# Kernel tuning notes

Measured on AMD Instinct MI355X. Metric: run time of the kernel, lower is better.

Reference implementation:

```python
import jax, jax.numpy as jnp
import numpy as np

H = 8        # num_heads
D = 128      # attention_dim
DV = 128     # linear_dim
B = 8
MAX_SEQLEN = 1024
LENGTHS = np.array([512 + 64 * b for b in range(B)], dtype=np.int64)  # jagged lengths
TOTAL = int(LENGTHS.sum())  # 5888


def setup_inputs() -> dict:
    key = jax.random.key(0)
    k1, k2, k3 = jax.random.split(key, 3)
    offsets = jnp.asarray(np.concatenate([[0], np.cumsum(LENGTHS)]), dtype=jnp.int32)
    tq = jax.random.normal(k1, (TOTAL, H * D), dtype=jnp.float32)
    tk = jax.random.normal(k2, (TOTAL, H * D), dtype=jnp.float32)
    tv = jax.random.normal(k3, (TOTAL, H * DV), dtype=jnp.float32)
    return {"tq": tq, "tk": tk, "tv": tv, "offsets": offsets,
            "max_seqlen": MAX_SEQLEN, "scaling_seqlen": -1}


def reference(tq, tk, tv, offsets, max_seqlen, scaling_seqlen):
    # HSTU jagged causal attention: out = (silu(q k^T * alpha) / n) @ v, per sequence.
    alpha = 1.0 / (D ** 0.5)
    denom = float(scaling_seqlen) if scaling_seqlen > 0 else float(max_seqlen)
    lengths = offsets[1:] - offsets[:-1]            # [B]
    pos = jnp.arange(max_seqlen, dtype=offsets.dtype)
    valid = pos[None, :] < lengths[:, None]          # [B, N] padding mask
    tok = offsets[:-1, None] + pos[None, :]          # [B, N] flat token index
    safe = jnp.where(valid, tok, 0)
    # gather jagged -> padded dense [B, N, H, D]
    q = tq.reshape(-1, H, D)[safe]
    k = tk.reshape(-1, H, D)[safe]
    v = tv.reshape(-1, H, DV)[safe]
    scores = jnp.einsum('bihd,bjhd->bhij', q, k) * alpha   # [B, H, N, N]
    attn = jax.nn.silu(scores) / denom                     # no softmax in HSTU
    causal = pos[:, None] >= pos[None, :]                  # attend to j <= i
    mask = causal[None, None, :, :] & valid[:, None, None, :] & valid[:, None, :, None]
    attn = jnp.where(mask, attn, 0.0)
    out = jnp.einsum('bhij,bjhd->bihd', attn, v)           # [B, N, H, DV]
    out = out * valid[:, :, None, None]
    # scatter padded -> jagged flat (invalid rows contribute zeros to index 0)
    flat = jnp.zeros((tq.shape[0], H, DV), tq.dtype).at[safe.reshape(-1)].add(
        out.reshape(-1, H, DV))
    return flat.reshape(-1, H * DV)
```

## Files before the change

kernel.cpp:

```cpp
#include <hip/hip_runtime.h>
#include <hip/hip_bf16.h>

typedef float f32x4 __attribute__((ext_vector_type(4)));
typedef __bf16 bf16x8 __attribute__((ext_vector_type(8)));
typedef unsigned int u32;
typedef unsigned int u32x2 __attribute__((ext_vector_type(2)));
typedef unsigned int u32x4 __attribute__((ext_vector_type(4)));
typedef unsigned short u16;

#define NH 8
#define HD 128
#define ROWE 1024
#define QB 64
#define JB 32
#define JCH 256
#define RSTRIDE 192
#define KSTR 148
#define VSTR 36
#define KSZ (JB*KSTR)
#define VSZ (HD*VSTR)

static __device__ __forceinline__ u16 bfb(float f) {
  return __builtin_bit_cast(u16, __float2bfloat16(f));
}
static __device__ __forceinline__ u32 pk2(float lo, float hi) {
  return (u32)bfb(lo) | ((u32)bfb(hi) << 16);
}

union FR { u32 u[4]; bf16x8 v; };

__global__ __launch_bounds__(256) void prep_cvt(
    const float* __restrict__ tk, const float* __restrict__ tv,
    u16* __restrict__ kb, u16* __restrict__ vb,
    float* __restrict__ outz, long n8)
{
  long idx = (long)blockIdx.x * 256 + threadIdx.x;
  long stride = (long)gridDim.x * 256;
  for (long i = idx; i < n8; i += stride) {
    const f32x4* kp = (const f32x4*)(tk + i * 8);
    const f32x4* vp = (const f32x4*)(tv + i * 8);
    f32x4 k0 = kp[0], k1 = kp[1], v0 = vp[0], v1 = vp[1];
    u32x4 ko, vo;
    ko.x = pk2(k0.x, k0.y); ko.y = pk2(k0.z, k0.w);
    ko.z = pk2(k1.x, k1.y); ko.w = pk2(k1.z, k1.w);
    vo.x = pk2(v0.x, v0.y); vo.y = pk2(v0.z, v0.w);
    vo.z = pk2(v1.x, v1.y); vo.w = pk2(v1.z, v1.w);
    *(u32x4*)(kb + i * 8) = ko;
    *(u32x4*)(vb + i * 8) = vo;
    f32x4 z = {0.f, 0.f, 0.f, 0.f};
    ((f32x4*)(outz + i * 8))[0] = z;
    ((f32x4*)(outz + i * 8))[1] = z;
  }
}

static __device__ __forceinline__ void unit_cj(int u, int& c, int& j) {
  c = (u & 3) | (((u >> 4) & 7) << 2);
  j = ((u >> 2) & 3) | (((u >> 7) & 7) << 2);
}

struct StReg { u32x2 k[4]; u32x2 v[4]; };

static __device__ __forceinline__ void stage_load(StReg& s,
    const u16* __restrict__ kb, const u16* __restrict__ vb,
    int base_row, int cap, int hoff, int tid) {
#pragma unroll
  for (int it = 0; it < 4; ++it) {
    int c, j; unit_cj(tid + (it << 8), c, j);
    int row = base_row + j; if (row > cap) row = cap;
    size_t g = (size_t)row * ROWE + hoff + 4 * c;
    s.k[it] = *(const u32x2*)(kb + g);
    s.v[it] = *(const u32x2*)(vb + g);
  }
}

static __device__ __forceinline__ void stage_write(const StReg& s,
    u16* kw, u16* vw, int tid) {
#pragma unroll
  for (int it = 0; it < 4; ++it) {
    int c, j; unit_cj(tid + (it << 8), c, j);
    *(u32x2*)(&kw[j * KSTR + 4 * c]) = s.k[it];
    u32x2 vv = s.v[it];
    vw[(4 * c + 0) * VSTR + j] = (u16)(vv.x);
    vw[(4 * c + 1) * VSTR + j] = (u16)(vv.x >> 16);
    vw[(4 * c + 2) * VSTR + j] = (u16)(vv.y);
    vw[(4 * c + 3) * VSTR + j] = (u16)(vv.y >> 16);
  }
}

__global__ __launch_bounds__(256, 3) void hstu_fwd(
    const u16* __restrict__ kb, const u16* __restrict__ vb,
    const float* __restrict__ tq, const int* __restrict__ offs,
    const int* __restrict__ pms, const int* __restrict__ pss,
    float* __restrict__ out, int nrows)
{
  __shared__ __align__(16) u16 kbuf[2][KSZ];
  __shared__ __align__(16) u16 vbuf[2][VSZ];

  const int h = blockIdx.x & 7;
  const int rblk = blockIdx.x >> 3;
  const int rstr = gridDim.x >> 3;

  int o[9];
#pragma unroll
  for (int i = 0; i < 9; ++i) o[i] = offs[i];

  const int cap = nrows - 1;
  const int tid = threadIdx.x;
  const int lane = tid & 63;
  const int w = tid >> 6;
  const int lrow = lane & 15;
  const int lgrp = lane >> 4;
  const int hoff = h * HD;

  const float qscale = 0.12751744f;
  int ms = pms[0], ss = pss[0];
  float den = (ss > 0) ? (float)ss : (float)ms;
  const float cs = 0.69314718056f / den;

  for (int e = rblk; ; e += rstr) {
    int r = e, selq = -1, selc = 0, soff = 0, sn = 0;
    for (int k = 15; k >= 0; --k) {
      for (int b = 0; b < 8; ++b) {
        int n = o[b + 1] - o[b];
        if (k * 64 >= n) continue;
        int je = k * 64 + 64; if (je > n) je = n;
        int nc = (je + JCH - 1) >> 8;
        if (r < nc) { selq = k; selc = r; soff = o[b]; sn = n; k = -1; break; }
        r -= nc;
      }
    }
    if (selq < 0) break;

    const int q0 = selq * QB;
    int jend = q0 + QB; if (jend > sn) jend = sn;
    const int ncq = (jend + JCH - 1) >> 8;
    const bool direct = (ncq == 1);
    const int j0c = selc * JCH;
    int jec = j0c + JCH; if (jec > jend) jec = jend;
    const int ntt = (jec - j0c + JB - 1) >> 5;

    FR qf[4];
    {
      int qr = soff + q0 + 16 * w + lrow; if (qr > cap) qr = cap;
      const float* qp = tq + (size_t)qr * ROWE + hoff;
#pragma unroll
      for (int ds = 0; ds < 4; ++ds) {
        f32x4 a = *(const f32x4*)(qp + ds * 32 + 4 * lgrp);
        f32x4 b = *(const f32x4*)(qp + ds * 32 + 4 * lgrp + 16);
        qf[ds].u[0] = pk2(a.x * qscale, a.y * qscale);
        qf[ds].u[1] = pk2(a.z * qscale, a.w * qscale);
        qf[ds].u[2] = pk2(b.x * qscale, b.y * qscale);
        qf[ds].u[3] = pk2(b.z * qscale, b.w * qscale);
      }
    }

    f32x4 acc[8];
#pragma unroll
    for (int i = 0; i < 8; ++i) acc[i] = (f32x4){0.f, 0.f, 0.f, 0.f};

    const int iq = q0 + 16 * w + lrow;

    __syncthreads();
    StReg st;
    stage_load(st, kb, vb, soff + j0c, cap, hoff, tid);
    stage_write(st, kbuf[0], vbuf[0], tid);

    for (int tt = 0; tt < ntt; ++tt) {
      __syncthreads();
      const bool pre = (tt + 1 < ntt);
      if (pre) stage_load(st, kb, vb, soff + j0c + (tt + 1) * JB, cap, hoff, tid);

      const int j0 = j0c + tt * JB;
      const int bsel = tt & 1;

      if (iq - lrow + 15 >= j0) {
        const char* kbc = (const char*)kbuf[bsel] + lrow * (2 * KSTR) + lgrp * 8;
        f32x4 s0 = {0.f, 0.f, 0.f, 0.f}, s1 = {0.f, 0.f, 0.f, 0.f};
#pragma unroll
        for (int ds = 0; ds < 4; ++ds) {
          FR a0, a1;
          const char* p = kbc + ds * 64;
          *(u32x2*)(&a0.u[0]) = *(const u32x2*)(p);
          *(u32x2*)(&a0.u[2]) = *(const u32x2*)(p + 32);
          *(u32x2*)(&a1.u[0]) = *(const u32x2*)(p + 16 * 2 * KSTR);
          *(u32x2*)(&a1.u[2]) = *(const u32x2*)(p + 16 * 2 * KSTR + 32);
          s0 = __builtin_amdgcn_mfma_f32_16x16x32_bf16(a0.v, qf[ds].v, s0, 0, 0, 0);
          s1 = __builtin_amdgcn_mfma_f32_16x16x32_bf16(a1.v, qf[ds].v, s1, 0, 0, 0);
        }

        const int jb0 = j0 + 4 * lgrp;
        float pv[8];
#pragma unroll
        for (int rr = 0; rr < 4; ++rr) {
          float y0 = s0[rr], y1 = s1[rr];
          float z0 = __fdividef(y0, 1.f + exp2f(-y0));
          float z1 = __fdividef(y1, 1.f + exp2f(-y1));
          pv[rr]     = (jb0 + rr      <= iq) ? z0 : 0.f;
          pv[rr + 4] = (jb0 + 16 + rr <= iq) ? z1 : 0.f;
        }
        FR pf;
        pf.u[0] = pk2(pv[0], pv[1]); pf.u[1] = pk2(pv[2], pv[3]);
        pf.u[2] = pk2(pv[4], pv[5]); pf.u[3] = pk2(pv[6], pv[7]);

        const char* vbc = (const char*)vbuf[bsel] + lrow * (2 * VSTR) + lgrp * 8;
#pragma unroll
        for (int sd = 0; sd < 8; ++sd) {
          FR vf;
          const char* p2 = vbc + sd * (16 * 2 * VSTR);
          *(u32x2*)(&vf.u[0]) = *(const u32x2*)(p2);
          *(u32x2*)(&vf.u[2]) = *(const u32x2*)(p2 + 32);
          acc[sd] = __builtin_amdgcn_mfma_f32_16x16x32_bf16(pf.v, vf.v, acc[sd], 0, 0, 0);
        }
      }
      if (pre) stage_write(st, kbuf[(tt + 1) & 1], vbuf[(tt + 1) & 1], tid);
    }

    const int or0 = q0 + 16 * w + 4 * lgrp;
#pragma unroll
    for (int rr = 0; rr < 4; ++rr) {
      int ir = or0 + rr;
      if (ir < sn) {
        float* op = out + (size_t)(soff + ir) * ROWE + hoff + lrow;
        if (direct) {
#pragma unroll
          for (int sd = 0; sd < 8; ++sd) op[sd * 16] = acc[sd][rr] * cs;
        } else {
#pragma unroll
          for (int sd = 0; sd < 8; ++sd)
            __hip_atomic_fetch_add(&op[sd * 16], acc[sd][rr] * cs,
                                   __ATOMIC_RELAXED, __HIP_MEMORY_SCOPE_AGENT);
        }
      }
    }
  }
}

extern "C" void kernel_launch(void* const* d_in, const int* in_sizes, int n_in,
                              void* d_out, int out_size, void* d_ws, size_t ws_size,
                              hipStream_t stream) {
  const float* tq = (const float*)d_in[0];
  const float* tk = (const float*)d_in[1];
  const float* tv = (const float*)d_in[2];
  const int* offs = (const int*)d_in[3];
  const int* pms  = (const int*)d_in[4];
  const int* pss  = (const int*)d_in[5];
  float* out = (float*)d_out;

  int nrows = in_sizes[0] / ROWE;
  u16* kbw = (u16*)d_ws;
  u16* vbw = kbw + (size_t)nrows * ROWE;
  long n8 = (long)nrows * ROWE / 8;

  hipLaunchKernelGGL(prep_cvt, dim3(2048), dim3(256), 0, stream,
                     tk, tv, kbw, vbw, out, n8);
  hipLaunchKernelGGL(hstu_fwd, dim3(NH * RSTRIDE), dim3(256), 0, stream,
                     kbw, vbw, tq, offs, pms, pss, out, nrows);
}
```

Baseline: 176.4 us.

## Use head-major K and transposed V, one wave per 16-row strip without LDS

The prep kernel now writes K in a head-major bf16 layout and V transposed per head (staged through LDS). It no longer zeroes the output. The attention kernel gives each wave its own 16-query strip, loads K and V fragments straight from global memory, and drops the LDS double-buffering, block barriers, the column-chunk split and the atomic accumulation. This removes synchronisation and atomics, but the four waves of a block no longer share K/V tiles, which raises global/L2 traffic and exposes load latency without explicit prefetch. It also assumes every sequence length is a multiple of 16.

```diff
diff --git a/kernel.cpp b/kernel.cpp
--- a/kernel.cpp
+++ b/kernel.cpp
@@ -11,14 +11,8 @@
 #define NH 8
 #define HD 128
 #define ROWE 1024
-#define QB 64
 #define JB 32
-#define JCH 256
-#define RSTRIDE 192
-#define KSTR 148
-#define VSTR 36
-#define KSZ (JB*KSTR)
-#define VSZ (HD*VSTR)
+#define VSTR2 72
 
 static __device__ __forceinline__ u16 bfb(float f) {
   return __builtin_bit_cast(u16, __float2bfloat16(f));
@@ -27,211 +21,166 @@
   return (u32)bfb(lo) | ((u32)bfb(hi) << 16);
 }
 
-union FR { u32 u[4]; bf16x8 v; };
+union FR { u32 u[4]; u32x4 q; bf16x8 v; };
 
 __global__ __launch_bounds__(256) void prep_cvt(
     const float* __restrict__ tk, const float* __restrict__ tv,
-    u16* __restrict__ kb, u16* __restrict__ vb,
-    float* __restrict__ outz, long n8)
+    u16* __restrict__ kb, u16* __restrict__ vt, int nrows)
 {
-  long idx = (long)blockIdx.x * 256 + threadIdx.x;
-  long stride = (long)gridDim.x * 256;
-  for (long i = idx; i < n8; i += stride) {
-    const f32x4* kp = (const f32x4*)(tk + i * 8);
-    const f32x4* vp = (const f32x4*)(tv + i * 8);
-    f32x4 k0 = kp[0], k1 = kp[1], v0 = vp[0], v1 = vp[1];
-    u32x4 ko, vo;
-    ko.x = pk2(k0.x, k0.y); ko.y = pk2(k0.z, k0.w);
-    ko.z = pk2(k1.x, k1.y); ko.w = pk2(k1.z, k1.w);
-    vo.x = pk2(v0.x, v0.y); vo.y = pk2(v0.z, v0.w);
-    vo.z = pk2(v1.x, v1.y); vo.w = pk2(v1.z, v1.w);
-    *(u32x4*)(kb + i * 8) = ko;
-    *(u32x4*)(vb + i * 8) = vo;
-    f32x4 z = {0.f, 0.f, 0.f, 0.f};
-    ((f32x4*)(outz + i * 8))[0] = z;
-    ((f32x4*)(outz + i * 8))[1] = z;
-  }
-}
-
-static __device__ __forceinline__ void unit_cj(int u, int& c, int& j) {
-  c = (u & 3) | (((u >> 4) & 7) << 2);
-  j = ((u >> 2) & 3) | (((u >> 7) & 7) << 2);
-}
-
-struct StReg { u32x2 k[4]; u32x2 v[4]; };
-
-static __device__ __forceinline__ void stage_load(StReg& s,
-    const u16* __restrict__ kb, const u16* __restrict__ vb,
-    int base_row, int cap, int hoff, int tid) {
+  __shared__ __align__(16) u16 vlds[HD * VSTR2];
+
+  const int h = blockIdx.x & 7;
+  const int tok0 = (blockIdx.x >> 3) * 64;
+  const int tid = threadIdx.x;
+  const int cap = nrows - 1;
+
+  u16* kbh = kb + (size_t)h * nrows * HD;
+  u16* vth = vt + (size_t)h * HD * nrows;
+
+#pragma unroll
+  for (int it = 0; it < 8; ++it) {
+    int u = tid + it * 256;
+    int tok = u >> 5, c = u & 31;
+    int row = tok0 + tok; if (row > cap) row = cap;
+    size_t g = (size_t)row * ROWE + h * HD + 4 * c;
+    f32x4 kv = *(const f32x4*)(tk + g);
+    f32x4 vv = *(const f32x4*)(tv + g);
+    u32x2 kp; kp.x = pk2(kv.x, kv.y); kp.y = pk2(kv.z, kv.w);
+    if (tok0 + tok <= cap)
+      *(u32x2*)(kbh + (size_t)(tok0 + tok) * HD + 4 * c) = kp;
+    vlds[(4 * c + 0) * VSTR2 + tok] = bfb(vv.x);
+    vlds[(4 * c + 1) * VSTR2 + tok] = bfb(vv.y);
+    vlds[(4 * c + 2) * VSTR2 + tok] = bfb(vv.z);
+    vlds[(4 * c + 3) * VSTR2 + tok] = bfb(vv.w);
+  }
+  __syncthreads();
 #pragma unroll
   for (int it = 0; it < 4; ++it) {
-    int c, j; unit_cj(tid + (it << 8), c, j);
-    int row = base_row + j; if (row > cap) row = cap;
-    size_t g = (size_t)row * ROWE + hoff + 4 * c;
-    s.k[it] = *(const u32x2*)(kb + g);
-    s.v[it] = *(const u32x2*)(vb + g);
-  }
-}
-
-static __device__ __forceinline__ void stage_write(const StReg& s,
-    u16* kw, u16* vw, int tid) {
-#pragma unroll
-  for (int it = 0; it < 4; ++it) {
-    int c, j; unit_cj(tid + (it << 8), c, j);
-    *(u32x2*)(&kw[j * KSTR + 4 * c]) = s.k[it];
-    u32x2 vv = s.v[it];
-    vw[(4 * c + 0) * VSTR + j] = (u16)(vv.x);
-    vw[(4 * c + 1) * VSTR + j] = (u16)(vv.x >> 16);
-    vw[(4 * c + 2) * VSTR + j] = (u16)(vv.y);
-    vw[(4 * c + 3) * VSTR + j] = (u16)(vv.y >> 16);
+    int u = tid + it * 256;
+    int dv = u >> 3, tch = u & 7;
+    u32x4 row = *(const u32x4*)(&vlds[dv * VSTR2 + tch * 8]);
+    int t0 = tok0 + tch * 8;
+    if (t0 + 7 <= cap)
+      *(u32x4*)(vth + (size_t)dv * nrows + t0) = row;
+    else {
+      const u16* s = (const u16*)&row;
+      for (int i = 0; i < 8 && t0 + i <= cap; ++i) vth[(size_t)dv * nrows + t0 + i] = s[i];
+    }
   }
 }
 
 __global__ __launch_bounds__(256, 3) void hstu_fwd(
-    const u16* __restrict__ kb, const u16* __restrict__ vb,
+    const u16* __restrict__ kb, const u16* __restrict__ vt,
     const float* __restrict__ tq, const int* __restrict__ offs,
     const int* __restrict__ pms, const int* __restrict__ pss,
     float* __restrict__ out, int nrows)
 {
-  __shared__ __align__(16) u16 kbuf[2][KSZ];
-  __shared__ __align__(16) u16 vbuf[2][VSZ];
-
   const int h = blockIdx.x & 7;
-  const int rblk = blockIdx.x >> 3;
-  const int rstr = gridDim.x >> 3;
-
-  int o[9];
-#pragma unroll
-  for (int i = 0; i < 9; ++i) o[i] = offs[i];
-
-  const int cap = nrows - 1;
+  const int r = blockIdx.x >> 3;
   const int tid = threadIdx.x;
   const int lane = tid & 63;
   const int w = tid >> 6;
   const int lrow = lane & 15;
   const int lgrp = lane >> 4;
-  const int hoff = h * HD;
+
+  int o[9];
+#pragma unroll
+  for (int i = 0; i < 9; ++i) o[i] = offs[i];
+
+  int want = r * 4 + w, selk = -1, soff = 0, sn = 0;
+  for (int k = 63; k >= 0; --k) {
+    for (int b = 0; b < 8; ++b) {
+      int n = o[b + 1] - o[b];
+      if (k * 16 < n) {
+        if (want == 0 && selk < 0) { selk = k; soff = o[b]; sn = n; }
+        --want;
+      }
+    }
+  }
+  if (selk < 0) return;
 
   const float qscale = 0.12751744f;
   int ms = pms[0], ss = pss[0];
   float den = (ss > 0) ? (float)ss : (float)ms;
   const float cs = 0.69314718056f / den;
 
-  for (int e = rblk; ; e += rstr) {
-    int r = e, selq = -1, selc = 0, soff = 0, sn = 0;
-    for (int k = 15; k >= 0; --k) {
-      for (int b = 0; b < 8; ++b) {
-        int n = o[b + 1] - o[b];
-        if (k * 64 >= n) continue;
-        int je = k * 64 + 64; if (je > n) je = n;
-        int nc = (je + JCH - 1) >> 8;
-        if (r < nc) { selq = k; selc = r; soff = o[b]; sn = n; k = -1; break; }
-        r -= nc;
-      }
-    }
-    if (selq < 0) break;
-
-    const int q0 = selq * QB;
-    int jend = q0 + QB; if (jend > sn) jend = sn;
-    const int ncq = (jend + JCH - 1) >> 8;
-    const bool direct = (ncq == 1);
-    const int j0c = selc * JCH;
-    int jec = j0c + JCH; if (jec > jend) jec = jend;
-    const int ntt = (jec - j0c + JB - 1) >> 5;
-
-    FR qf[4];
-    {
-      int qr = soff + q0 + 16 * w + lrow; if (qr > cap) qr = cap;
-      const float* qp = tq + (size_t)qr * ROWE + hoff;
-#pragma unroll
-      for (int ds = 0; ds < 4; ++ds) {
-        f32x4 a = *(const f32x4*)(qp + ds * 32 + 4 * lgrp);
-        f32x4 b = *(const f32x4*)(qp + ds * 32 + 4 * lgrp + 16);
-        qf[ds].u[0] = pk2(a.x * qscale, a.y * qscale);
-        qf[ds].u[1] = pk2(a.z * qscale, a.w * qscale);
-        qf[ds].u[2] = pk2(b.x * qscale, b.y * qscale);
-        qf[ds].u[3] = pk2(b.z * qscale, b.w * qscale);
-      }
-    }
-
-    f32x4 acc[8];
-#pragma unroll
-    for (int i = 0; i < 8; ++i) acc[i] = (f32x4){0.f, 0.f, 0.f, 0.f};
-
-    const int iq = q0 + 16 * w + lrow;
-
-    __syncthreads();
-    StReg st;
-    stage_load(st, kb, vb, soff + j0c, cap, hoff, tid);
-    stage_write(st, kbuf[0], vbuf[0], tid);
-
-    for (int tt = 0; tt < ntt; ++tt) {
-      __syncthreads();
-      const bool pre = (tt + 1 < ntt);
-      if (pre) stage_load(st, kb, vb, soff + j0c + (tt + 1) * JB, cap, hoff, tid);
-
-      const int j0 = j0c + tt * JB;
-      const int bsel = tt & 1;
-
-      if (iq - lrow + 15 >= j0) {
-        const char* kbc = (const char*)kbuf[bsel] + lrow * (2 * KSTR) + lgrp * 8;
-        f32x4 s0 = {0.f, 0.f, 0.f, 0.f}, s1 = {0.f, 0.f, 0.f, 0.f};
-#pragma unroll
-        for (int ds = 0; ds < 4; ++ds) {
-          FR a0, a1;
-          const char* p = kbc + ds * 64;
-          *(u32x2*)(&a0.u[0]) = *(const u32x2*)(p);
-          *(u32x2*)(&a0.u[2]) = *(const u32x2*)(p + 32);
-          *(u32x2*)(&a1.u[0]) = *(const u32x2*)(p + 16 * 2 * KSTR);
-          *(u32x2*)(&a1.u[2]) = *(const u32x2*)(p + 16 * 2 * KSTR + 32);
-          s0 = __builtin_amdgcn_mfma_f32_16x16x32_bf16(a0.v, qf[ds].v, s0, 0, 0, 0);
-          s1 = __builtin_amdgcn_mfma_f32_16x16x32_bf16(a1.v, qf[ds].v, s1, 0, 0, 0);
-        }
-
-        const int jb0 = j0 + 4 * lgrp;
-        float pv[8];
-#pragma unroll
-        for (int rr = 0; rr < 4; ++rr) {
-          float y0 = s0[rr], y1 = s1[rr];
-          float z0 = __fdividef(y0, 1.f + exp2f(-y0));
-          float z1 = __fdividef(y1, 1.f + exp2f(-y1));
-          pv[rr]     = (jb0 + rr      <= iq) ? z0 : 0.f;
-          pv[rr + 4] = (jb0 + 16 + rr <= iq) ? z1 : 0.f;
-        }
-        FR pf;
-        pf.u[0] = pk2(pv[0], pv[1]); pf.u[1] = pk2(pv[2], pv[3]);
-        pf.u[2] = pk2(pv[4], pv[5]); pf.u[3] = pk2(pv[6], pv[7]);
-
-        const char* vbc = (const char*)vbuf[bsel] + lrow * (2 * VSTR) + lgrp * 8;
-#pragma unroll
-        for (int sd = 0; sd < 8; ++sd) {
-          FR vf;
-          const char* p2 = vbc + sd * (16 * 2 * VSTR);
-          *(u32x2*)(&vf.u[0]) = *(const u32x2*)(p2);
-          *(u32x2*)(&vf.u[2]) = *(const u32x2*)(p2 + 32);
-          acc[sd] = __builtin_amdgcn_mfma_f32_16x16x32_bf16(pf.v, vf.v, acc[sd], 0, 0, 0);
-        }
-      }
-      if (pre) stage_write(st, kbuf[(tt + 1) & 1], vbuf[(tt + 1) & 1], tid);
-    }
-
-    const int or0 = q0 + 16 * w + 4 * lgrp;
+  const int q0 = selk * 16;
+  const int iq = q0 + lrow;
+
+  FR qf[4];
+  {
+    const float* qp = tq + (size_t)(soff + q0 + lrow) * ROWE + h * HD;
+#pragma unroll
+    for (int ds = 0; ds < 4; ++ds) {
+      f32x4 a = *(const f32x4*)(qp + ds * 32 + lgrp * 8);
+      f32x4 b = *(const f32x4*)(qp + ds * 32 + lgrp * 8 + 4);
+      qf[ds].u[0] = pk2(a.x * qscale, a.y * qscale);
+      qf[ds].u[1] = pk2(a.z * qscale, a.w * qscale);
+      qf[ds].u[2] = pk2(b.x * qscale, b.y * qscale);
+      qf[ds].u[3] = pk2(b.z * qscale, b.w * qscale);
+    }
+  }
+
+  const u16* kbh = kb + (size_t)h * nrows * HD;
+  const u16* vth = vt + (size_t)h * HD * nrows;
+
+  f32x4 acc[8];
+#pragma unroll
+  for (int i = 0; i < 8; ++i) acc[i] = (f32x4){0.f, 0.f, 0.f, 0.f};
+
+  const int ntj = (selk >> 1) + 1;
+
+  for (int tt = 0; tt < ntj; ++tt) {
+    const int j0 = tt * JB;
+
+    const u16* k0p = kbh + (size_t)(soff + j0 + lrow) * HD + lgrp * 8;
+    const u16* k1p = k0p + 16 * HD;
+    FR a0[4], a1[4];
+#pragma unroll
+    for (int ds = 0; ds < 4; ++ds) {
+      a0[ds].q = *(const u32x4*)(k0p + ds * 32);
+      a1[ds].q = *(const u32x4*)(k1p + ds * 32);
+    }
+    FR vf[8];
+#pragma unroll
+    for (int sd = 0; sd < 8; ++sd) {
+      const u16* vp = vth + (size_t)(sd * 16 + lrow) * nrows + soff + j0 + 4 * lgrp;
+      *(u32x2*)(&vf[sd].u[0]) = *(const u32x2*)(vp);
+      *(u32x2*)(&vf[sd].u[2]) = *(const u32x2*)(vp + 16);
+    }
+
+    f32x4 s0 = {0.f, 0.f, 0.f, 0.f}, s1 = {0.f, 0.f, 0.f, 0.f};
+#pragma unroll
+    for (int ds = 0; ds < 4; ++ds) {
+      s0 = __builtin_amdgcn_mfma_f32_16x16x32_bf16(a0[ds].v, qf[ds].v, s0, 0, 0, 0);
+      s1 = __builtin_amdgcn_mfma_f32_16x16x32_bf16(a1[ds].v, qf[ds].v, s1, 0, 0, 0);
+    }
+
+    const int jb0 = j0 + 4 * lgrp;
+    float pv[8];
 #pragma unroll
     for (int rr = 0; rr < 4; ++rr) {
-      int ir = or0 + rr;
-      if (ir < sn) {
-        float* op = out + (size_t)(soff + ir) * ROWE + hoff + lrow;
-        if (direct) {
-#pragma unroll
-          for (int sd = 0; sd < 8; ++sd) op[sd * 16] = acc[sd][rr] * cs;
-        } else {
-#pragma unroll
-          for (int sd = 0; sd < 8; ++sd)
-            __hip_atomic_fetch_add(&op[sd * 16], acc[sd][rr] * cs,
-                                   __ATOMIC_RELAXED, __HIP_MEMORY_SCOPE_AGENT);
-        }
-      }
-    }
+      float y0 = s0[rr], y1 = s1[rr];
+      float z0 = __fdividef(y0, 1.f + exp2f(-y0));
+      float z1 = __fdividef(y1, 1.f + exp2f(-y1));
+      pv[rr]     = (jb0 + rr      <= iq) ? z0 : 0.f;
+      pv[rr + 4] = (jb0 + 16 + rr <= iq) ? z1 : 0.f;
+    }
+    FR pf;
+    pf.u[0] = pk2(pv[0], pv[1]); pf.u[1] = pk2(pv[2], pv[3]);
+    pf.u[2] = pk2(pv[4], pv[5]); pf.u[3] = pk2(pv[6], pv[7]);
+
+#pragma unroll
+    for (int sd = 0; sd < 8; ++sd)
+      acc[sd] = __builtin_amdgcn_mfma_f32_16x16x32_bf16(pf.v, vf[sd].v, acc[sd], 0, 0, 0);
+  }
+
+#pragma unroll
+  for (int rr = 0; rr < 4; ++rr) {
+    int ir = q0 + 4 * lgrp + rr;
+    float* op = out + (size_t)(soff + ir) * ROWE + h * HD + lrow;
+#pragma unroll
+    for (int sd = 0; sd < 8; ++sd) op[sd * 16] = acc[sd][rr] * cs;
   }
 }
 
@@ -248,11 +197,15 @@
 
   int nrows = in_sizes[0] / ROWE;
   u16* kbw = (u16*)d_ws;
-  u16* vbw = kbw + (size_t)nrows * ROWE;
-  long n8 = (long)nrows * ROWE / 8;
-
-  hipLaunchKernelGGL(prep_cvt, dim3(2048), dim3(256), 0, stream,
-                     tk, tv, kbw, vbw, out, n8);
-  hipLaunchKernelGGL(hstu_fwd, dim3(NH * RSTRIDE), dim3(256), 0, stream,
-                     kbw, vbw, tq, offs, pms, pss, out, nrows);
-}
+  u16* vbt = kbw + (size_t)nrows * ROWE;
+
+  int tokblks = (nrows + 63) / 64;
+  hipLaunchKernelGGL(prep_cvt, dim3(NH * tokblks), dim3(256), 0, stream,
+                     tk, tv, kbw, vbt, nrows);
+
+  int nstrips = 0;
+  nstrips = nrows / 16 + 8;
+  int blocks = (nstrips + 3) / 4;
+  hipLaunchKernelGGL(hstu_fwd, dim3(NH * blocks), dim3(256), 0, stream,
+                     kbw, vbt, tq, offs, pms, pss, out, nrows);
+}
```

Result: slower. 272.8 us (+54.7%).
